# Performance work log

Measured on AMD Instinct MI355X. Metric: run time of the kernel, lower is better.

The kernel has to match this reference:

```python
import jax, jax.numpy as jnp
import numpy as np

EPS = float(np.finfo(np.float32).eps)


def fake_quant_w(w):
    # per-output-channel symmetric int8 fake quant; w: (out, in)
    w_d = jax.lax.stop_gradient(w)
    max_abs = jnp.max(jnp.abs(w_d), axis=1, keepdims=True)
    scale = jnp.maximum(max_abs / 127.0, EPS)
    w_q = jnp.clip(jnp.round(w_d / scale), -127, 127)
    return w_q * scale


def woq_linear(x, w, b):
    return x @ fake_quant_w(w).T + b


def setup_inputs() -> dict:
    key = jax.random.key(0)
    ks = jax.random.split(key, 9)
    dim = 1024
    B, S = 2, 2048
    def wmat(k):
        return jax.random.normal(k, (dim, dim), dtype=jnp.float32) * (1.0 / np.sqrt(dim))
    def bvec(k):
        return jax.random.normal(k, (dim,), dtype=jnp.float32) * 0.01
    return {
        "x": jax.random.normal(ks[0], (B, S, dim), dtype=jnp.float32),
        "wq": wmat(ks[1]), "bq": bvec(ks[2]),
        "wk": wmat(ks[3]), "bk": bvec(ks[4]),
        "wv": wmat(ks[5]), "bv": bvec(ks[6]),
        "wp": wmat(ks[7]), "bp": bvec(ks[8]),
    }


def reference(x, wq, bq, wk, bk, wv, bv, wp, bp):
    B, S, C = x.shape
    H = 16
    D = C // H
    scale = D ** -0.5
    # QKV projections with fake-quantized weights -> (B, H, S, D)
    q = woq_linear(x, wq, bq).reshape(B, S, H, D).transpose(0, 2, 1, 3)
    k = woq_linear(x, wk, bk).reshape(B, S, H, D).transpose(0, 2, 1, 3)
    v = woq_linear(x, wv, bv).reshape(B, S, H, D).transpose(0, 2, 1, 3)
    attn = jnp.einsum("bhsd,bhtd->bhst", q, k) * scale  # (B,H,S,S)
    attn = jax.nn.softmax(attn, axis=-1)
    out = jnp.einsum("bhst,bhtd->bhsd", attn, v)
    out = out.transpose(0, 2, 1, 3).reshape(B, S, C)
    return woq_linear(out, wp, bp)
```

## Files before the change

kernel.cpp:

```cpp
#include <hip/hip_runtime.h>
#include <stdint.h>

typedef short bf16x8 __attribute__((ext_vector_type(8)));
typedef float f32x4 __attribute__((ext_vector_type(4)));
typedef uint16_t u16;
typedef uint32_t u32;
typedef u16 u16x4 __attribute__((ext_vector_type(4)));

#define EPSF 1.1920929e-07f

static __device__ __forceinline__ u16 f2bf(float f) {
  union { float f; uint32_t u; } v; v.f = f;
  return (u16)((v.u + 0x7FFFu + ((v.u >> 16) & 1u)) >> 16);
}
static __device__ __forceinline__ float bf2f(u16 h) {
  union { uint32_t u; float f; } v; v.u = ((uint32_t)h) << 16;
  return v.f;
}
static __device__ __forceinline__ float exp2_fast(float x) {
  return __builtin_amdgcn_exp2f(x);
}
static __device__ __forceinline__ u32 cvt_pk_bf16(float lo, float hi) {
  u32 r;
  asm("v_cvt_pk_bf16_f32 %0, %1, %2" : "=v"(r) : "v"(lo), "v"(hi));
  return r;
}
static __device__ __forceinline__ void gload_lds16(const void* g, void* l) {
  __builtin_amdgcn_global_load_lds(
      (const __attribute__((address_space(1))) void*)g,
      (__attribute__((address_space(3))) void*)l, 16, 0, 0);
}
template <int N>
static __device__ __forceinline__ void vmwait() {
  asm volatile("s_waitcnt vmcnt(%0)" ::"i"(N) : "memory");
}

__global__ __launch_bounds__(256) void prep_kernel(
    const float* __restrict__ wq, const float* __restrict__ wk,
    const float* __restrict__ wv, const float* __restrict__ wp,
    const float* __restrict__ x,
    u16* __restrict__ wout, float* __restrict__ scales, u16* __restrict__ xb) {
  const int t = threadIdx.x;
  if (blockIdx.x < 4096) {
    const int row = blockIdx.x & 1023;
    const int mat = blockIdx.x >> 10;
    const float* W = (mat == 0) ? wq : (mat == 1) ? wk : (mat == 2) ? wv : wp;
    const float4 v = ((const float4*)(W + (size_t)row * 1024))[t];
    float m = fmaxf(fmaxf(fabsf(v.x), fabsf(v.y)), fmaxf(fabsf(v.z), fabsf(v.w)));
#pragma unroll
    for (int off = 1; off < 64; off <<= 1) m = fmaxf(m, __shfl_xor(m, off));
    __shared__ float red[4];
    if ((t & 63) == 0) red[t >> 6] = m;
    __syncthreads();
    m = fmaxf(fmaxf(red[0], red[1]), fmaxf(red[2], red[3]));
    const float scale = fmaxf(m / 127.0f, EPSF);
    float q0 = fminf(fmaxf(rintf(v.x / scale), -127.f), 127.f);
    float q1 = fminf(fmaxf(rintf(v.y / scale), -127.f), 127.f);
    float q2 = fminf(fmaxf(rintf(v.z / scale), -127.f), 127.f);
    float q3 = fminf(fmaxf(rintf(v.w / scale), -127.f), 127.f);
    u16x4 o; o.x = f2bf(q0); o.y = f2bf(q1); o.z = f2bf(q2); o.w = f2bf(q3);
    *(u16x4*)(wout + ((size_t)(mat * 1024 + row)) * 1024 + t * 4) = o;
    if (t == 0) scales[mat * 1024 + row] = scale;
  } else {
    const int i = (blockIdx.x - 4096) * 256 + t;
    const float4 v = ((const float4*)x)[i];
    u16x4 hv;
    hv.x = f2bf(v.x); hv.y = f2bf(v.y); hv.z = f2bf(v.z); hv.w = f2bf(v.w);
    *(u16x4*)(xb + (size_t)i * 4) = hv;
  }
}

template <int MODE, int MR, int NR, int NT, int KT, int LDA>
__global__ __launch_bounds__(512) void gemm_kernel(
    const u16* __restrict__ A, const u16* __restrict__ Bw,
    const float* __restrict__ scales, const float* __restrict__ b0,
    const float* __restrict__ b1, const float* __restrict__ b2,
    u16* __restrict__ qkv, float* __restrict__ outp) {
  constexpr int BM = 2 * MR * 16;
  constexpr int BN = 4 * NR * 16;
  constexpr int OPS = BM / 64 + BN / 64;
  __shared__ u16 As[2][BM * 64];
  __shared__ u16 Bs[2][BN * 64];
  const int tid = threadIdx.x;
  const int w = tid >> 6, l = tid & 63;
  const int per = gridDim.x >> 3;
  const int L = (blockIdx.x & 7) * per + (blockIdx.x >> 3);
  const int tile_n = (L % NT) * BN;
  const int tile_m = (L / NT) * BM;
  const int wm = w >> 2, wn = w & 3;
  const int l15 = l & 15, l4 = l >> 4;
  const int sw = l15 & 7;

  f32x4 acc[MR][NR];
  const f32x4 vzero = {0.f, 0.f, 0.f, 0.f};
#pragma unroll
  for (int m = 0; m < MR; ++m)
#pragma unroll
    for (int n = 0; n < NR; ++n) acc[m][n] = vzero;

  const int r8 = tid >> 3;
  const int g = tid & 7;
  const int gs = g ^ (r8 & 7);
  auto STAGE = [&](int slot, int j) {
    const int kb = j * 64;
    const int kbB = kb & 1023;
#pragma unroll
    for (int i = 0; i < BM / 64; ++i)
      gload_lds16(A + (size_t)(tile_m + i * 64 + r8) * LDA + kb + gs * 8,
                  &As[slot][(i * 64 + r8) * 64 + g * 8]);
#pragma unroll
    for (int i = 0; i < BN / 64; ++i)
      gload_lds16(Bw + (size_t)(tile_n + i * 64 + r8) * 1024 + kbB + gs * 8,
                  &Bs[slot][(i * 64 + r8) * 64 + g * 8]);
  };

  STAGE(0, 0);
  STAGE(1, 1);
  vmwait<OPS>();
  __builtin_amdgcn_s_barrier();

  for (int j = 0; j < KT; ++j) {
    const int cur = j & 1;
#pragma unroll
    for (int ks = 0; ks < 2; ++ks) {
      bf16x8 af[MR], bfv[NR];
      const int sg8 = ((ks * 4 + l4) ^ sw) * 8;
#pragma unroll
      for (int m = 0; m < MR; ++m)
        af[m] = *(const bf16x8*)(&As[cur][(wm * (MR * 16) + m * 16 + l15) * 64 + sg8]);
#pragma unroll
      for (int n = 0; n < NR; ++n)
        bfv[n] = *(const bf16x8*)(&Bs[cur][(wn * (NR * 16) + n * 16 + l15) * 64 + sg8]);
      __builtin_amdgcn_s_setprio(1);
#pragma unroll
      for (int m = 0; m < MR; ++m)
#pragma unroll
        for (int n = 0; n < NR; ++n)
          acc[m][n] = __builtin_amdgcn_mfma_f32_16x16x32_bf16(af[m], bfv[n], acc[m][n], 0, 0, 0);
      __builtin_amdgcn_s_setprio(0);
    }
    __builtin_amdgcn_s_barrier();
    if (j + 2 < KT) {
      STAGE(cur, j + 2);
      vmwait<OPS>();
    } else {
      vmwait<0>();
    }
    __builtin_amdgcn_s_barrier();
  }

#pragma unroll
  for (int m = 0; m < MR; ++m) {
#pragma unroll
    for (int n = 0; n < NR; ++n) {
      const int col = tile_n + wn * (NR * 16) + n * 16 + l15;
      const float sc = scales[col];
      if constexpr (MODE == 0) {
        const int mat = col >> 10, oo = col & 1023;
        const float* bias = (mat == 0) ? b0 : (mat == 1) ? b1 : b2;
        const float bb = bias[oo];
        const int hh = oo >> 6, dd = oo & 63;
        if (mat == 2) {
          const int rowm0 = tile_m + wm * (MR * 16) + m * 16 + l4 * 4;
          const int b = rowm0 >> 11, s = rowm0 & 2047;
          u16x4 pk;
#pragma unroll
          for (int jj = 0; jj < 4; ++jj) pk[jj] = f2bf(acc[m][n][jj] * sc + bb);
          *(u16x4*)(qkv + (size_t)2 * 4194304 +
                    ((size_t)(b * 16 + hh) * 64 + dd) * 2048 + s) = pk;
        } else {
#pragma unroll
          for (int jj = 0; jj < 4; ++jj) {
            const int rowm = tile_m + wm * (MR * 16) + m * 16 + l4 * 4 + jj;
            const int b = rowm >> 11, s = rowm & 2047;
            float y = acc[m][n][jj] * sc + bb;
            if (mat == 0) y *= 0.18033688011112042f;
            qkv[(size_t)mat * 4194304 + ((size_t)(b * 16 + hh) * 2048 + s) * 64 + dd] = f2bf(y);
          }
        }
      } else {
        const float bb = b0[col];
#pragma unroll
        for (int jj = 0; jj < 4; ++jj) {
          const int rowm = tile_m + wm * (MR * 16) + m * 16 + l4 * 4 + jj;
          outp[(size_t)rowm * 1024 + col] = acc[m][n][jj] * sc + bb;
        }
      }
    }
  }
}

__global__ __launch_bounds__(512) void attn_kernel(
    const u16* __restrict__ qg, const u16* __restrict__ kg,
    const u16* __restrict__ vtg, u16* __restrict__ po) {
  __shared__ u16 Kt[2][128 * 64];
  __shared__ u16 Vt[2][64 * 128];
  __shared__ u16 Pl[8 * 16 * 64];
  const int tid = threadIdx.x;
  const int w = tid >> 6, l = tid & 63;
  const int Lb = (blockIdx.x & 7) * 64 + (blockIdx.x >> 3);
  const int bh = Lb >> 4;
  const int qt = Lb & 15;
  const u16* qp = qg + (size_t)bh * 131072;
  const u16* kp = kg + (size_t)bh * 131072;
  const u16* vp = vtg + (size_t)bh * 131072;
  const int qrow0 = qt * 128 + w * 16;
  const int l15 = l & 15, l4 = l >> 4;
  const int sw = l15 & 7;

  auto STAGE = [&](int slot, int kt) {
#pragma unroll
    for (int i = 0; i < 2; ++i) {
      const int rk = i * 64 + (tid >> 3);
      gload_lds16(kp + (size_t)(kt + rk) * 64 + (((tid & 7) ^ (rk & 7)) << 3),
                  &Kt[slot][i * 4096 + tid * 8]);
    }
#pragma unroll
    for (int i = 0; i < 2; ++i) {
      const int rv = i * 32 + (tid >> 4);
      gload_lds16(vp + (size_t)rv * 2048 + kt + (((tid & 15) ^ (rv & 7)) << 3),
                  &Vt[slot][i * 4096 + tid * 8]);
    }
  };

  bf16x8 qf[2];
#pragma unroll
  for (int dk = 0; dk < 2; ++dk)
    qf[dk] = *(const bf16x8*)(qp + (size_t)(qrow0 + l15) * 64 + dk * 32 + l4 * 8);

  const f32x4 vzero = {0.f, 0.f, 0.f, 0.f};
  f32x4 O[4];
#pragma unroll
  for (int di = 0; di < 4; ++di) O[di] = vzero;
  float lrun = 0.f;

  STAGE(0, 0);
  STAGE(1, 128);
  vmwait<4>();
  __builtin_amdgcn_s_barrier();

  for (int j = 0; j < 16; ++j) {
    const int cur = j & 1;

    f32x4 sfr[8];
#pragma unroll
    for (int ki = 0; ki < 8; ++ki) sfr[ki] = vzero;
#pragma unroll
    for (int dk = 0; dk < 2; ++dk) {
      bf16x8 kf[8];
#pragma unroll
      for (int ki = 0; ki < 8; ++ki)
        kf[ki] = *(const bf16x8*)(&Kt[cur][(ki * 16 + l15) * 64 + (((dk * 4 + l4) ^ sw) << 3)]);
      __builtin_amdgcn_s_setprio(1);
#pragma unroll
      for (int ki = 0; ki < 8; ++ki)
        sfr[ki] = __builtin_amdgcn_mfma_f32_16x16x32_bf16(kf[ki], qf[dk], sfr[ki], 0, 0, 0);
      __builtin_amdgcn_s_setprio(0);
    }

#pragma unroll
    for (int half = 0; half < 2; ++half) {
      float rs = 0.f;
      u32 pw[8];
#pragma unroll
      for (int ki = 0; ki < 4; ++ki) {
        const f32x4 s4 = sfr[half * 4 + ki];
        const float p0 = exp2_fast(s4[0]);
        const float p1 = exp2_fast(s4[1]);
        const float p2 = exp2_fast(s4[2]);
        const float p3 = exp2_fast(s4[3]);
        rs += (p0 + p1) + (p2 + p3);
        pw[ki * 2 + 0] = cvt_pk_bf16(p0, p1);
        pw[ki * 2 + 1] = cvt_pk_bf16(p2, p3);
      }
      lrun += rs;

      u32* pb = (u32*)Pl + w * 512 + l15 * 32;
#pragma unroll
      for (int ki = 0; ki < 4; ++ki) {
#pragma unroll
        for (int h = 0; h < 2; ++h) {
          const int W = ki * 8 + l4 * 2 + h;
          pb[(((W >> 2) ^ sw) << 2) + (W & 3)] = pw[ki * 2 + h];
        }
      }

#pragma unroll
      for (int kkl = 0; kkl < 2; ++kkl) {
        const bf16x8 pf =
            *(const bf16x8*)(Pl + w * 1024 + l15 * 64 + (((kkl * 4 + l4) ^ sw) << 3));
        bf16x8 vf[4];
#pragma unroll
        for (int di = 0; di < 4; ++di)
          vf[di] = *(const bf16x8*)(&Vt[cur][(di * 16 + l15) * 128 +
                                             (((half * 8 + kkl * 4 + l4) ^ sw) << 3)]);
        __builtin_amdgcn_s_setprio(1);
#pragma unroll
        for (int di = 0; di < 4; ++di)
          O[di] = __builtin_amdgcn_mfma_f32_16x16x32_bf16(pf, vf[di], O[di], 0, 0, 0);
        __builtin_amdgcn_s_setprio(0);
      }
    }

    __builtin_amdgcn_s_barrier();
    if (j + 2 < 16) {
      STAGE(cur, (j + 2) * 128);
      vmwait<4>();
    } else {
      vmwait<0>();
    }
    __builtin_amdgcn_s_barrier();
  }

  lrun += __shfl_xor(lrun, 16);
  lrun += __shfl_xor(lrun, 32);
  const int b = bh >> 4, hh = bh & 15;
  float lq[4];
#pragma unroll
  for (int jj = 0; jj < 4; ++jj)
    lq[jj] = __builtin_amdgcn_rcpf(__shfl(lrun, l4 * 4 + jj));
#pragma unroll
  for (int di = 0; di < 4; ++di)
#pragma unroll
    for (int jj = 0; jj < 4; ++jj) {
      const float oval = O[di][jj] * lq[jj];
      const int srw = qrow0 + l4 * 4 + jj;
      const int c = hh * 64 + di * 16 + l15;
      const u16 hi = f2bf(oval);
      const u16 lo = f2bf(oval - bf2f(hi));
      const size_t base = ((size_t)(b * 2048 + srw)) * 2048;
      po[base + c] = hi;
      po[base + 1024 + c] = lo;
    }
}

extern "C" void kernel_launch(void* const* d_in, const int* in_sizes, int n_in,
                              void* d_out, int out_size, void* d_ws, size_t ws_size,
                              hipStream_t stream) {
  (void)in_sizes; (void)n_in; (void)out_size; (void)ws_size;
  const float* x  = (const float*)d_in[0];
  const float* wq = (const float*)d_in[1];
  const float* bq = (const float*)d_in[2];
  const float* wk = (const float*)d_in[3];
  const float* bk = (const float*)d_in[4];
  const float* wv = (const float*)d_in[5];
  const float* bv = (const float*)d_in[6];
  const float* wp = (const float*)d_in[7];
  const float* bp = (const float*)d_in[8];

  char* ws = (char*)d_ws;
  u16*   wquant = (u16*)ws;
  float* scales = (float*)(ws + 8388608);
  u16*   xb     = (u16*)(ws + 8404992);
  u16*   po     = xb;
  u16*   qkv    = (u16*)(ws + 25182208);

  prep_kernel<<<dim3(8192), dim3(256), 0, stream>>>(
      wq, wk, wv, wp, x, wquant, scales, xb);
  gemm_kernel<0, 4, 3, 16, 16, 1024><<<dim3(512), dim3(512), 0, stream>>>(
      xb, wquant, scales, bq, bk, bv, qkv, nullptr);
  attn_kernel<<<dim3(512), dim3(512), 0, stream>>>(
      qkv, qkv + 4194304, qkv + 8388608, po);
  gemm_kernel<1, 2, 2, 8, 32, 2048><<<dim3(512), dim3(512), 0, stream>>>(
      po, wquant + 3145728, scales + 3072, bp, nullptr, nullptr, nullptr, (float*)d_out);
}
```

Before: 118.2 us.

## Process two query tiles per wave in attention and drop split-bf16 output

The attention kernel now runs 4 waves per block, each handling 32 query rows as two 16-row fragments. Each K/V fragment read from shared memory is reused across two MFMAs, and staging uses more loads per thread. The attention output is also written as a single bf16 value instead of a hi/lo bf16 pair, so the output projection GEMM uses K=1024 instead of 2048. This halves the projection GEMM work and output traffic, at the cost of lower precision in the projected input and higher register pressure in attention.

Measured after the change: 104.9 us. -11.3%, faster.

```diff
diff --git a/kernel.cpp b/kernel.cpp
--- a/kernel.cpp
+++ b/kernel.cpp
@@ -190,12 +190,12 @@
   }
 }
 
-__global__ __launch_bounds__(512) void attn_kernel(
+__global__ __launch_bounds__(256) void attn_kernel(
     const u16* __restrict__ qg, const u16* __restrict__ kg,
     const u16* __restrict__ vtg, u16* __restrict__ po) {
   __shared__ u16 Kt[2][128 * 64];
   __shared__ u16 Vt[2][64 * 128];
-  __shared__ u16 Pl[8 * 16 * 64];
+  __shared__ u16 Pl[4 * 2 * 16 * 64];
   const int tid = threadIdx.x;
   const int w = tid >> 6, l = tid & 63;
   const int Lb = (blockIdx.x & 7) * 64 + (blockIdx.x >> 3);
@@ -204,47 +204,54 @@
   const u16* qp = qg + (size_t)bh * 131072;
   const u16* kp = kg + (size_t)bh * 131072;
   const u16* vp = vtg + (size_t)bh * 131072;
-  const int qrow0 = qt * 128 + w * 16;
+  const int qrow0 = qt * 128 + w * 32;
   const int l15 = l & 15, l4 = l >> 4;
   const int sw = l15 & 7;
 
   auto STAGE = [&](int slot, int kt) {
 #pragma unroll
-    for (int i = 0; i < 2; ++i) {
-      const int rk = i * 64 + (tid >> 3);
+    for (int i = 0; i < 4; ++i) {
+      const int rk = i * 32 + (tid >> 3);
       gload_lds16(kp + (size_t)(kt + rk) * 64 + (((tid & 7) ^ (rk & 7)) << 3),
-                  &Kt[slot][i * 4096 + tid * 8]);
-    }
-#pragma unroll
-    for (int i = 0; i < 2; ++i) {
-      const int rv = i * 32 + (tid >> 4);
+                  &Kt[slot][i * 2048 + tid * 8]);
+    }
+#pragma unroll
+    for (int i = 0; i < 4; ++i) {
+      const int rv = i * 16 + (tid >> 4);
       gload_lds16(vp + (size_t)rv * 2048 + kt + (((tid & 15) ^ (rv & 7)) << 3),
-                  &Vt[slot][i * 4096 + tid * 8]);
+                  &Vt[slot][i * 2048 + tid * 8]);
     }
   };
 
-  bf16x8 qf[2];
+  bf16x8 qfr[2][2];
 #pragma unroll
   for (int dk = 0; dk < 2; ++dk)
-    qf[dk] = *(const bf16x8*)(qp + (size_t)(qrow0 + l15) * 64 + dk * 32 + l4 * 8);
+#pragma unroll
+    for (int qf = 0; qf < 2; ++qf)
+      qfr[dk][qf] =
+          *(const bf16x8*)(qp + (size_t)(qrow0 + qf * 16 + l15) * 64 + dk * 32 + l4 * 8);
 
   const f32x4 vzero = {0.f, 0.f, 0.f, 0.f};
-  f32x4 O[4];
-#pragma unroll
-  for (int di = 0; di < 4; ++di) O[di] = vzero;
-  float lrun = 0.f;
+  f32x4 O[4][2];
+#pragma unroll
+  for (int di = 0; di < 4; ++di)
+#pragma unroll
+    for (int qf = 0; qf < 2; ++qf) O[di][qf] = vzero;
+  float lrun[2] = {0.f, 0.f};
 
   STAGE(0, 0);
   STAGE(1, 128);
-  vmwait<4>();
+  vmwait<8>();
   __builtin_amdgcn_s_barrier();
 
   for (int j = 0; j < 16; ++j) {
     const int cur = j & 1;
 
-    f32x4 sfr[8];
-#pragma unroll
-    for (int ki = 0; ki < 8; ++ki) sfr[ki] = vzero;
+    f32x4 sfr[2][8];
+#pragma unroll
+    for (int qf = 0; qf < 2; ++qf)
+#pragma unroll
+      for (int ki = 0; ki < 8; ++ki) sfr[qf][ki] = vzero;
 #pragma unroll
     for (int dk = 0; dk < 2; ++dk) {
       bf16x8 kf[8];
@@ -254,41 +261,51 @@
       __builtin_amdgcn_s_setprio(1);
 #pragma unroll
       for (int ki = 0; ki < 8; ++ki)
-        sfr[ki] = __builtin_amdgcn_mfma_f32_16x16x32_bf16(kf[ki], qf[dk], sfr[ki], 0, 0, 0);
+#pragma unroll
+        for (int qf = 0; qf < 2; ++qf)
+          sfr[qf][ki] = __builtin_amdgcn_mfma_f32_16x16x32_bf16(kf[ki], qfr[dk][qf], sfr[qf][ki], 0, 0, 0);
       __builtin_amdgcn_s_setprio(0);
     }
 
 #pragma unroll
     for (int half = 0; half < 2; ++half) {
-      float rs = 0.f;
-      u32 pw[8];
-#pragma unroll
-      for (int ki = 0; ki < 4; ++ki) {
-        const f32x4 s4 = sfr[half * 4 + ki];
-        const float p0 = exp2_fast(s4[0]);
-        const float p1 = exp2_fast(s4[1]);
-        const float p2 = exp2_fast(s4[2]);
-        const float p3 = exp2_fast(s4[3]);
-        rs += (p0 + p1) + (p2 + p3);
-        pw[ki * 2 + 0] = cvt_pk_bf16(p0, p1);
-        pw[ki * 2 + 1] = cvt_pk_bf16(p2, p3);
-      }
-      lrun += rs;
-
-      u32* pb = (u32*)Pl + w * 512 + l15 * 32;
-#pragma unroll
-      for (int ki = 0; ki < 4; ++ki) {
-#pragma unroll
-        for (int h = 0; h < 2; ++h) {
-          const int W = ki * 8 + l4 * 2 + h;
-          pb[(((W >> 2) ^ sw) << 2) + (W & 3)] = pw[ki * 2 + h];
+      u32 pw[2][8];
+#pragma unroll
+      for (int qf = 0; qf < 2; ++qf) {
+        float rs = 0.f;
+#pragma unroll
+        for (int ki = 0; ki < 4; ++ki) {
+          const f32x4 s4 = sfr[qf][half * 4 + ki];
+          const float p0 = exp2_fast(s4[0]);
+          const float p1 = exp2_fast(s4[1]);
+          const float p2 = exp2_fast(s4[2]);
+          const float p3 = exp2_fast(s4[3]);
+          rs += (p0 + p1) + (p2 + p3);
+          pw[qf][ki * 2 + 0] = cvt_pk_bf16(p0, p1);
+          pw[qf][ki * 2 + 1] = cvt_pk_bf16(p2, p3);
         }
+        lrun[qf] += rs;
+      }
+#pragma unroll
+      for (int qf = 0; qf < 2; ++qf) {
+        u32* pb = (u32*)Pl + (w * 2 + qf) * 512 + l15 * 32;
+#pragma unroll
+        for (int ki = 0; ki < 4; ++ki) {
+#pragma unroll
+          for (int h = 0; h < 2; ++h) {
+            const int W = ki * 8 + l4 * 2 + h;
+            pb[(((W >> 2) ^ sw) << 2) + (W & 3)] = pw[qf][ki * 2 + h];
+          }
+        }
       }
 
 #pragma unroll
       for (int kkl = 0; kkl < 2; ++kkl) {
-        const bf16x8 pf =
-            *(const bf16x8*)(Pl + w * 1024 + l15 * 64 + (((kkl * 4 + l4) ^ sw) << 3));
+        bf16x8 pf[2];
+#pragma unroll
+        for (int qf = 0; qf < 2; ++qf)
+          pf[qf] = *(const bf16x8*)(Pl + (w * 2 + qf) * 1024 + l15 * 64 +
+                                    (((kkl * 4 + l4) ^ sw) << 3));
         bf16x8 vf[4];
 #pragma unroll
         for (int di = 0; di < 4; ++di)
@@ -297,7 +314,9 @@
         __builtin_amdgcn_s_setprio(1);
 #pragma unroll
         for (int di = 0; di < 4; ++di)
-          O[di] = __builtin_amdgcn_mfma_f32_16x16x32_bf16(pf, vf[di], O[di], 0, 0, 0);
+#pragma unroll
+          for (int qf = 0; qf < 2; ++qf)
+            O[di][qf] = __builtin_amdgcn_mfma_f32_16x16x32_bf16(pf[qf], vf[di], O[di][qf], 0, 0, 0);
         __builtin_amdgcn_s_setprio(0);
       }
     }
@@ -305,33 +324,35 @@
     __builtin_amdgcn_s_barrier();
     if (j + 2 < 16) {
       STAGE(cur, (j + 2) * 128);
-      vmwait<4>();
+      vmwait<8>();
     } else {
       vmwait<0>();
     }
     __builtin_amdgcn_s_barrier();
   }
 
-  lrun += __shfl_xor(lrun, 16);
-  lrun += __shfl_xor(lrun, 32);
   const int b = bh >> 4, hh = bh & 15;
-  float lq[4];
-#pragma unroll
-  for (int jj = 0; jj < 4; ++jj)
-    lq[jj] = __builtin_amdgcn_rcpf(__shfl(lrun, l4 * 4 + jj));
-#pragma unroll
-  for (int di = 0; di < 4; ++di)
-#pragma unroll
-    for (int jj = 0; jj < 4; ++jj) {
-      const float oval = O[di][jj] * lq[jj];
-      const int srw = qrow0 + l4 * 4 + jj;
-      const int c = hh * 64 + di * 16 + l15;
-      const u16 hi = f2bf(oval);
-      const u16 lo = f2bf(oval - bf2f(hi));
-      const size_t base = ((size_t)(b * 2048 + srw)) * 2048;
-      po[base + c] = hi;
-      po[base + 1024 + c] = lo;
-    }
+#pragma unroll
+  for (int qf = 0; qf < 2; ++qf) {
+    lrun[qf] += __shfl_xor(lrun[qf], 16);
+    lrun[qf] += __shfl_xor(lrun[qf], 32);
+  }
+#pragma unroll
+  for (int qf = 0; qf < 2; ++qf) {
+    float lq[4];
+#pragma unroll
+    for (int jj = 0; jj < 4; ++jj)
+      lq[jj] = __builtin_amdgcn_rcpf(__shfl(lrun[qf], l4 * 4 + jj));
+#pragma unroll
+    for (int di = 0; di < 4; ++di)
+#pragma unroll
+      for (int jj = 0; jj < 4; ++jj) {
+        const float oval = O[di][qf][jj] * lq[jj];
+        const int srw = qrow0 + qf * 16 + l4 * 4 + jj;
+        const int c = hh * 64 + di * 16 + l15;
+        po[((size_t)(b * 2048 + srw)) * 1024 + c] = f2bf(oval);
+      }
+  }
 }
 
 extern "C" void kernel_launch(void* const* d_in, const int* in_sizes, int n_in,
@@ -359,8 +380,8 @@
       wq, wk, wv, wp, x, wquant, scales, xb);
   gemm_kernel<0, 4, 3, 16, 16, 1024><<<dim3(512), dim3(512), 0, stream>>>(
       xb, wquant, scales, bq, bk, bv, qkv, nullptr);
-  attn_kernel<<<dim3(512), dim3(512), 0, stream>>>(
+  attn_kernel<<<dim3(512), dim3(256), 0, stream>>>(
       qkv, qkv + 4194304, qkv + 8388608, po);
-  gemm_kernel<1, 2, 2, 8, 32, 2048><<<dim3(512), dim3(512), 0, stream>>>(
+  gemm_kernel<1, 2, 2, 8, 16, 1024><<<dim3(512), dim3(512), 0, stream>>>(
       po, wquant + 3145728, scales + 3072, bp, nullptr, nullptr, nullptr, (float*)d_out);
 }
```
